# Performance work log

Measured on AMD Instinct MI355X. Metric: run time of the kernel, lower is better.

## Reference

```python
import jax, jax.numpy as jnp
import numpy as np

B, N, C, W = 64, 4096, 128, 64
WIN = N - W + 1  # 4033, length of each sliding-filter input
BN_EPS = 1e-5


def setup_inputs() -> dict:
    key = jax.random.key(0)
    ks = jax.random.split(key, 8)
    s_in = 1.0 / np.sqrt(WIN)   # nn.Linear default init scale
    s_2 = 1.0 / np.sqrt(2.0)
    s_out = 1.0 / np.sqrt(W)
    return {
        "x": jax.random.normal(ks[0], (B, N, C, 2), dtype=jnp.float32),
        "w_in_real": jax.random.normal(ks[1], (C, WIN), dtype=jnp.float32) * s_in,
        "w_in_imag": jax.random.normal(ks[2], (C, WIN), dtype=jnp.float32) * s_in,
        "A_nonlin": jax.random.normal(ks[3], (C, 2, 2), dtype=jnp.float32) * s_2,
        "Wc": jax.random.normal(ks[4], (2, 2), dtype=jnp.float32) * s_2,
        "w_out_real": jax.random.normal(ks[5], (C, W), dtype=jnp.float32) * s_out,
        "w_out_imag": jax.random.normal(ks[6], (C, W), dtype=jnp.float32) * s_out,
        "bn_gamma": jnp.ones((C,), dtype=jnp.float32),
        "bn_beta": jnp.zeros((C,), dtype=jnp.float32),
    }


def _depthwise_corr(sig, w):
    # sig: [B, N, C], w: [C, K] -> [B, N-K+1, C]
    # filtered[b, t, c] = sum_k sig[b, t+k, c] * w[c, k]  (matches per-channel Linear on slices)
    rhs = w.T[:, None, :]  # [K, 1, C]
    return jax.lax.conv_general_dilated(
        sig, rhs, window_strides=(1,), padding="VALID",
        dimension_numbers=("NWC", "WIO", "NWC"),
        feature_group_count=sig.shape[-1])


def reference(x, w_in_real, w_in_imag, A_nonlin, Wc, w_out_real, w_out_imag, bn_gamma, bn_beta):
    xr, xi = x[..., 0], x[..., 1]               # [B, N, C]
    # --- per-channel sliding input filters (out_window positions) ---
    fr = _depthwise_corr(xr, w_in_real)          # [B, W, C]
    fi = _depthwise_corr(xi, w_in_imag)          # [B, W, C]
    v = jnp.stack([fr, fi], axis=-1)             # [B, W, C, 2]
    # --- per-channel 2x2 linear: out_j = sum_i A[c, j, i] * v_i ---
    u = jnp.einsum("bwci,cji->bwcj", v, A_nonlin)
    amp = jnp.sum(u * u, axis=-1, keepdims=True)  # r^2 + i^2
    u = amp * u
    # --- shared 2x2 coeff linear ---
    u = jnp.einsum("bwci,ji->bwcj", u, Wc)
    # --- per-channel output filters over the out_window axis ---
    out_r = jnp.einsum("bwc,cw->bc", u[..., 0], w_out_real)
    out_i = jnp.einsum("bwc,cw->bc", u[..., 1], w_out_imag)
    out = jnp.stack([out_r, out_i], axis=-1)     # [B, C, 2]
    # --- BatchNorm1d(C), training-mode batch statistics over (B, last) dims ---
    mean = jnp.mean(out, axis=(0, 2), keepdims=True)
    var = jnp.mean((out - mean) ** 2, axis=(0, 2), keepdims=True)
    out = (out - mean) * jax.lax.rsqrt(var + BN_EPS)
    return out * bn_gamma[None, :, None] + bn_beta[None, :, None]
```

## Files before the change

### kernel.cpp

```cpp
#include <hip/hip_runtime.h>

typedef float v2f __attribute__((ext_vector_type(2)));
typedef float v4f __attribute__((ext_vector_type(4)));

#define B_ 64
#define N_ 4096
#define C_ 128
#define W_ 64
#define WIN_ 4033
#define CG 16
#define NCHUNK 256
#define KPAD 4176
#define WSTRIDE 338

__global__ void prep_w(const float* __restrict__ wr, const float* __restrict__ wi,
                       v2f* __restrict__ w2pad) {
  int idx = blockIdx.x * 256 + threadIdx.x;
  int c = idx / KPAD;
  int kk = idx - c * KPAD;
  int k = kk - 64;
  v2f v = {0.f, 0.f};
  if (k >= 0 && k < WIN_) {
    v.x = wr[c * WIN_ + k];
    v.y = wi[c * WIN_ + k];
  }
  w2pad[idx] = v;
}

__global__ __launch_bounds__(256, 2) void conv_main(
    const v2f* __restrict__ x2,
    const v2f* __restrict__ w2pad,
    const float* __restrict__ Anl,
    const float* __restrict__ Wcm,
    const float* __restrict__ wor,
    const float* __restrict__ woi,
    float* __restrict__ pre) {
  __shared__ __attribute__((aligned(16))) v2f wsh[CG * WSTRIDE];

  int tid = threadIdx.x;
  int bb = blockIdx.x >> 3;
  int cg = blockIdx.x & 7;
  int cbase = cg * CG;
  int cl = (tid >> 2) & 15;
  int t0g = tid & 3;
  int np = tid >> 6;
  int t0 = t0g << 4;
  int nbase = np << 6;

  v2f zero = {0.f, 0.f};
  v2f acc[16];
#pragma unroll
  for (int i = 0; i < 16; i++) acc[i] = zero;

  const v2f* xg = x2 + (size_t)bb * N_ * C_ + cbase + cl;
  const v2f* wrow = wsh + cl * WSTRIDE;

  for (int n0 = 0; n0 < N_; n0 += NCHUNK) {
    {
      const v4f* wsrc = (const v4f*)(w2pad + (size_t)cbase * KPAD + n0);
      v4f* wdst = (v4f*)wsh;
      for (int i = tid; i < CG * 168; i += 256) {
        int c = i / 168;
        int u = i - c * 168;
        wdst[c * 169 + u] = wsrc[(size_t)c * (KPAD / 2) + u];
      }
    }
    __syncthreads();

    v2f wA[16], wB[16], xA[16], xB[16];
#pragma unroll
    for (int m = 0; m < 16; m++) wA[m] = wrow[nbase + 48 - t0 + m];
#pragma unroll
    for (int j = 0; j < 16; j++) xA[j] = xg[(size_t)(n0 + nbase + j) * C_];

    auto pref = [&](int nb, v2f* xv) {
#pragma unroll
      for (int j = 0; j < 16; j++) xv[j] = xg[(size_t)(n0 + nb + j) * C_];
    };
    auto do16 = [&](int nb, const v2f* xv, const v2f* wold, v2f* wnew) {
#pragma unroll
      for (int j = 0; j < 16; j++) wnew[j] = wrow[nb + 64 - t0 + j];
#pragma unroll
      for (int j = 0; j < 16; j++) {
#pragma unroll
        for (int i = 0; i < 16; i++) {
          int e = j - i;
          v2f wv = (e < 0) ? wold[16 + e] : wnew[e];
          acc[i] = __builtin_elementwise_fma(xv[j], wv, acc[i]);
        }
      }
    };

    pref(nbase + 16, xB);
    do16(nbase + 0, xA, wA, wB);
    pref(nbase + 32, xA);
    do16(nbase + 16, xB, wB, wA);
    pref(nbase + 48, xB);
    do16(nbase + 32, xA, wA, wB);
    do16(nbase + 48, xB, wB, wA);
    __syncthreads();
  }

  v2f* fpart = wsh;
#pragma unroll
  for (int i = 0; i < 16; i++) fpart[((np * CG + cl) << 6) + t0 + i] = acc[i];
  __syncthreads();

  int cl2 = tid & 15;
  int tq = tid >> 4;
  int c = cbase + cl2;
  float a00 = Anl[c * 4 + 0], a01 = Anl[c * 4 + 1];
  float a10 = Anl[c * 4 + 2], a11 = Anl[c * 4 + 3];
  float wc00 = Wcm[0], wc01 = Wcm[1], wc10 = Wcm[2], wc11 = Wcm[3];
  float or_ = 0.f, oi_ = 0.f;
#pragma unroll
  for (int q = 0; q < 4; q++) {
    int t = tq + (q << 4);
    v2f f = fpart[(0 * CG + cl2) * 64 + t] + fpart[(1 * CG + cl2) * 64 + t] +
            fpart[(2 * CG + cl2) * 64 + t] + fpart[(3 * CG + cl2) * 64 + t];
    float ur = a00 * f.x + a01 * f.y;
    float ui = a10 * f.x + a11 * f.y;
    float amp = ur * ur + ui * ui;
    ur *= amp;
    ui *= amp;
    float vr = wc00 * ur + wc01 * ui;
    float vi = wc10 * ur + wc11 * ui;
    or_ += vr * wor[c * 64 + t];
    oi_ += vi * woi[c * 64 + t];
  }
  or_ += __shfl_down(or_, 16, 64);
  oi_ += __shfl_down(oi_, 16, 64);
  or_ += __shfl_down(or_, 32, 64);
  oi_ += __shfl_down(oi_, 32, 64);
  __syncthreads();
  v2f* opart = wsh;
  if ((tid & 63) < 16) {
    v2f t = {or_, oi_};
    opart[(tid >> 6) * 16 + cl2] = t;
  }
  __syncthreads();
  if (tid < 16) {
    v2f r = opart[cl2] + opart[16 + cl2] + opart[32 + cl2] + opart[48 + cl2];
    pre[((size_t)bb * C_ + cbase + cl2) * 2 + 0] = r.x;
    pre[((size_t)bb * C_ + cbase + cl2) * 2 + 1] = r.y;
  }
}

__global__ void bn_kernel(const float* __restrict__ pre, const float* __restrict__ gamma,
                          const float* __restrict__ beta, float* __restrict__ out) {
  int c = blockIdx.x, tid = threadIdx.x;
  int b = tid >> 1, comp = tid & 1;
  float v = pre[((size_t)b * C_ + c) * 2 + comp];
  float s = v, s2 = v * v;
#pragma unroll
  for (int d = 32; d > 0; d >>= 1) {
    s += __shfl_down(s, d, 64);
    s2 += __shfl_down(s2, d, 64);
  }
  __shared__ float red[4];
  if ((tid & 63) == 0) {
    red[(tid >> 6) * 2 + 0] = s;
    red[(tid >> 6) * 2 + 1] = s2;
  }
  __syncthreads();
  float sum = red[0] + red[2], sumsq = red[1] + red[3];
  float mean = sum * 0.0078125f;
  float var = sumsq * 0.0078125f - mean * mean;
  float inv = rsqrtf(var + 1e-5f);
  out[((size_t)b * C_ + c) * 2 + comp] = (v - mean) * inv * gamma[c] + beta[c];
}

extern "C" void kernel_launch(void* const* d_in, const int* in_sizes, int n_in,
                              void* d_out, int out_size, void* d_ws, size_t ws_size,
                              hipStream_t stream) {
  (void)in_sizes; (void)n_in; (void)out_size; (void)ws_size;
  const float* x   = (const float*)d_in[0];
  const float* wir = (const float*)d_in[1];
  const float* wii = (const float*)d_in[2];
  const float* Anl = (const float*)d_in[3];
  const float* Wcm = (const float*)d_in[4];
  const float* wrr = (const float*)d_in[5];
  const float* wri = (const float*)d_in[6];
  const float* gam = (const float*)d_in[7];
  const float* bet = (const float*)d_in[8];

  v2f* w2pad = (v2f*)d_ws;
  float* pre = (float*)((char*)d_ws + (size_t)C_ * KPAD * sizeof(v2f));

  prep_w<<<(C_ * KPAD) / 256, 256, 0, stream>>>(wir, wii, w2pad);
  conv_main<<<B_ * (C_ / CG), 256, 0, stream>>>((const v2f*)x, w2pad, Anl, Wcm,
                                                wrr, wri, pre);
  bn_kernel<<<C_, 128, 0, stream>>>(pre, gam, bet, (float*)d_out);
}
```

Measured before the change: 496.2 us.

## Split convolution over sequence halves and move nonlinearity into separate kernel

Splits the sequence dimension of the depthwise correlation across two blocks per (batch, channel-group), doubling grid size to 1024 blocks, and halves the shared weight chunk so occupancy can rise to 4 blocks per CU. Thread mapping changes so channel is the fastest index, aiming at more coalesced x loads. Partial filter outputs are reduced in shared memory and written to a workspace. A new nonlin_out kernel then sums the two halves and applies the nonlinearity and output filter. This costs an extra launch, an intermediate global round-trip, and tighter register limits.

```diff
diff --git a/kernel.cpp b/kernel.cpp
--- a/kernel.cpp
+++ b/kernel.cpp
@@ -1,7 +1,6 @@
 #include <hip/hip_runtime.h>
 
 typedef float v2f __attribute__((ext_vector_type(2)));
-typedef float v4f __attribute__((ext_vector_type(4)));
 
 #define B_ 64
 #define N_ 4096
@@ -9,9 +8,11 @@
 #define W_ 64
 #define WIN_ 4033
 #define CG 16
-#define NCHUNK 256
+#define NCHUNK 128
+#define NSPLIT 2
 #define KPAD 4176
-#define WSTRIDE 338
+#define WROW 192
+#define WSTRIDE 193
 
 __global__ void prep_w(const float* __restrict__ wr, const float* __restrict__ wi,
                        v2f* __restrict__ w2pad) {
@@ -27,25 +28,23 @@
   w2pad[idx] = v;
 }
 
-__global__ __launch_bounds__(256, 2) void conv_main(
+__global__ __launch_bounds__(256, 4) void conv_main(
     const v2f* __restrict__ x2,
     const v2f* __restrict__ w2pad,
-    const float* __restrict__ Anl,
-    const float* __restrict__ Wcm,
-    const float* __restrict__ wor,
-    const float* __restrict__ woi,
-    float* __restrict__ pre) {
+    v2f* __restrict__ fq) {
   __shared__ __attribute__((aligned(16))) v2f wsh[CG * WSTRIDE];
 
   int tid = threadIdx.x;
-  int bb = blockIdx.x >> 3;
-  int cg = blockIdx.x & 7;
+  int bid = blockIdx.x;
+  int cg = bid & 7;
+  int bb = (bid >> 3) & 63;
+  int ns = bid >> 9;
   int cbase = cg * CG;
-  int cl = (tid >> 2) & 15;
-  int t0g = tid & 3;
+  int cl = tid & 15;
+  int t0g = (tid >> 4) & 3;
   int np = tid >> 6;
   int t0 = t0g << 4;
-  int nbase = np << 6;
+  int nbase = np << 5;
 
   v2f zero = {0.f, 0.f};
   v2f acc[16];
@@ -55,69 +54,96 @@
   const v2f* xg = x2 + (size_t)bb * N_ * C_ + cbase + cl;
   const v2f* wrow = wsh + cl * WSTRIDE;
 
-  for (int n0 = 0; n0 < N_; n0 += NCHUNK) {
+  int nstart = ns * (N_ / NSPLIT);
+  int nend = nstart + N_ / NSPLIT;
+
+  v2f wA[16], wB[16], xA[16], xB[16];
+#pragma unroll
+  for (int j = 0; j < 16; j++) xA[j] = xg[(size_t)(nstart + nbase + j) * C_];
+
+  auto do16 = [&](int nb, const v2f* xv, const v2f* wold, v2f* wnew) {
+#pragma unroll
+    for (int j = 0; j < 16; j++) wnew[j] = wrow[nb + 64 - t0 + j];
+#pragma unroll
+    for (int j = 0; j < 16; j++) {
+#pragma unroll
+      for (int i = 0; i < 16; i++) {
+        int e = j - i;
+        v2f wv = (e < 0) ? wold[16 + e] : wnew[e];
+        acc[i] = __builtin_elementwise_fma(xv[j], wv, acc[i]);
+      }
+    }
+  };
+
+  for (int n0 = nstart; n0 < nend; n0 += NCHUNK) {
     {
-      const v4f* wsrc = (const v4f*)(w2pad + (size_t)cbase * KPAD + n0);
-      v4f* wdst = (v4f*)wsh;
-      for (int i = tid; i < CG * 168; i += 256) {
-        int c = i / 168;
-        int u = i - c * 168;
-        wdst[c * 169 + u] = wsrc[(size_t)c * (KPAD / 2) + u];
+      const v2f* wsrc = w2pad + (size_t)cbase * KPAD + n0;
+#pragma unroll
+      for (int k = 0; k < 12; k++) {
+        int i = tid + k * 256;
+        int c = i / WROW;
+        int u = i - c * WROW;
+        wsh[c * WSTRIDE + u] = wsrc[(size_t)c * KPAD + u];
       }
     }
     __syncthreads();
 
-    v2f wA[16], wB[16], xA[16], xB[16];
 #pragma unroll
     for (int m = 0; m < 16; m++) wA[m] = wrow[nbase + 48 - t0 + m];
 #pragma unroll
-    for (int j = 0; j < 16; j++) xA[j] = xg[(size_t)(n0 + nbase + j) * C_];
-
-    auto pref = [&](int nb, v2f* xv) {
-#pragma unroll
-      for (int j = 0; j < 16; j++) xv[j] = xg[(size_t)(n0 + nb + j) * C_];
-    };
-    auto do16 = [&](int nb, const v2f* xv, const v2f* wold, v2f* wnew) {
-#pragma unroll
-      for (int j = 0; j < 16; j++) wnew[j] = wrow[nb + 64 - t0 + j];
-#pragma unroll
-      for (int j = 0; j < 16; j++) {
-#pragma unroll
-        for (int i = 0; i < 16; i++) {
-          int e = j - i;
-          v2f wv = (e < 0) ? wold[16 + e] : wnew[e];
-          acc[i] = __builtin_elementwise_fma(xv[j], wv, acc[i]);
-        }
-      }
-    };
-
-    pref(nbase + 16, xB);
+    for (int j = 0; j < 16; j++) xB[j] = xg[(size_t)(n0 + nbase + 16 + j) * C_];
+
     do16(nbase + 0, xA, wA, wB);
-    pref(nbase + 32, xA);
+
+    if (n0 + NCHUNK < nend) {
+#pragma unroll
+      for (int j = 0; j < 16; j++) xA[j] = xg[(size_t)(n0 + NCHUNK + nbase + j) * C_];
+    }
+
     do16(nbase + 16, xB, wB, wA);
-    pref(nbase + 48, xB);
-    do16(nbase + 32, xA, wA, wB);
-    do16(nbase + 48, xB, wB, wA);
     __syncthreads();
   }
 
   v2f* fpart = wsh;
-#pragma unroll
-  for (int i = 0; i < 16; i++) fpart[((np * CG + cl) << 6) + t0 + i] = acc[i];
-  __syncthreads();
-
-  int cl2 = tid & 15;
-  int tq = tid >> 4;
-  int c = cbase + cl2;
+  if (np >= 2) {
+#pragma unroll
+    for (int i = 0; i < 16; i++) fpart[(np - 2) * 1040 + cl * 65 + t0 + i] = acc[i];
+  }
+  __syncthreads();
+  if (np < 2) {
+#pragma unroll
+    for (int i = 0; i < 16; i++) acc[i] += fpart[np * 1040 + cl * 65 + t0 + i];
+  }
+  __syncthreads();
+  if (np == 1) {
+#pragma unroll
+    for (int i = 0; i < 16; i++) fpart[cl * 65 + t0 + i] = acc[i];
+  }
+  __syncthreads();
+  if (np == 0) {
+    v2f* out = fq + (size_t)(ns * B_ + bb) * 64 * C_ + cbase + cl;
+#pragma unroll
+    for (int i = 0; i < 16; i++) {
+      v2f r = acc[i] + fpart[cl * 65 + t0 + i];
+      out[(size_t)(t0 + i) * C_] = r;
+    }
+  }
+}
+
+__global__ void nonlin_out(const v2f* __restrict__ fq, const float* __restrict__ Anl,
+                           const float* __restrict__ Wcm, const float* __restrict__ wor,
+                           const float* __restrict__ woi, v2f* __restrict__ pre) {
+  int b = blockIdx.x;
+  int c = threadIdx.x;
   float a00 = Anl[c * 4 + 0], a01 = Anl[c * 4 + 1];
   float a10 = Anl[c * 4 + 2], a11 = Anl[c * 4 + 3];
   float wc00 = Wcm[0], wc01 = Wcm[1], wc10 = Wcm[2], wc11 = Wcm[3];
+  const v2f* f0 = fq + (size_t)b * 64 * C_ + c;
+  const v2f* f1 = fq + (size_t)(B_ + b) * 64 * C_ + c;
   float or_ = 0.f, oi_ = 0.f;
-#pragma unroll
-  for (int q = 0; q < 4; q++) {
-    int t = tq + (q << 4);
-    v2f f = fpart[(0 * CG + cl2) * 64 + t] + fpart[(1 * CG + cl2) * 64 + t] +
-            fpart[(2 * CG + cl2) * 64 + t] + fpart[(3 * CG + cl2) * 64 + t];
+#pragma unroll 4
+  for (int t = 0; t < 64; t++) {
+    v2f f = f0[(size_t)t * C_] + f1[(size_t)t * C_];
     float ur = a00 * f.x + a01 * f.y;
     float ui = a10 * f.x + a11 * f.y;
     float amp = ur * ur + ui * ui;
@@ -128,22 +154,8 @@
     or_ += vr * wor[c * 64 + t];
     oi_ += vi * woi[c * 64 + t];
   }
-  or_ += __shfl_down(or_, 16, 64);
-  oi_ += __shfl_down(oi_, 16, 64);
-  or_ += __shfl_down(or_, 32, 64);
-  oi_ += __shfl_down(oi_, 32, 64);
-  __syncthreads();
-  v2f* opart = wsh;
-  if ((tid & 63) < 16) {
-    v2f t = {or_, oi_};
-    opart[(tid >> 6) * 16 + cl2] = t;
-  }
-  __syncthreads();
-  if (tid < 16) {
-    v2f r = opart[cl2] + opart[16 + cl2] + opart[32 + cl2] + opart[48 + cl2];
-    pre[((size_t)bb * C_ + cbase + cl2) * 2 + 0] = r.x;
-    pre[((size_t)bb * C_ + cbase + cl2) * 2 + 1] = r.y;
-  }
+  v2f r = {or_, oi_};
+  pre[(size_t)b * C_ + c] = r;
 }
 
 __global__ void bn_kernel(const float* __restrict__ pre, const float* __restrict__ gamma,
@@ -185,10 +197,11 @@
   const float* bet = (const float*)d_in[8];
 
   v2f* w2pad = (v2f*)d_ws;
-  float* pre = (float*)((char*)d_ws + (size_t)C_ * KPAD * sizeof(v2f));
+  v2f* fq = (v2f*)((char*)d_ws + (size_t)C_ * KPAD * sizeof(v2f));
+  v2f* pre = (v2f*)((char*)fq + (size_t)NSPLIT * B_ * 64 * C_ * sizeof(v2f));
 
   prep_w<<<(C_ * KPAD) / 256, 256, 0, stream>>>(wir, wii, w2pad);
-  conv_main<<<B_ * (C_ / CG), 256, 0, stream>>>((const v2f*)x, w2pad, Anl, Wcm,
-                                                wrr, wri, pre);
-  bn_kernel<<<C_, 128, 0, stream>>>(pre, gam, bet, (float*)d_out);
-}
+  conv_main<<<B_ * 8 * NSPLIT, 256, 0, stream>>>((const v2f*)x, w2pad, fq);
+  nonlin_out<<<B_, C_, 0, stream>>>(fq, Anl, Wcm, wrr, wri, pre);
+  bn_kernel<<<C_, 128, 0, stream>>>((const float*)pre, gam, bet, (float*)d_out);
+}
```

New measurement: 1.082 ms. 118% more time.
